# Performance work log

Hardware: AMD Instinct MI355X
Metric: run time of the kernel (lower is better)

Reference implementation:

```python
import jax, jax.numpy as jnp
import numpy as np


def setup_inputs() -> dict:
    key = jax.random.key(0)
    k1, k2, k3 = jax.random.split(key, 3)
    B, H, S, D = 2, 16, 2048, 64
    q = jax.random.normal(k1, (B, H, S, D), dtype=jnp.float32)
    k = jax.random.normal(k2, (B, H, S, D), dtype=jnp.float32)
    v = jax.random.normal(k3, (B, H, S, D), dtype=jnp.float32)
    return {"q": q, "k": k, "v": v}


def reference(q, k, v):
    orig_dtype = q.dtype
    q = q.astype(jnp.float32)
    k = k.astype(jnp.float32)
    v = v.astype(jnp.float32)
    B, H, S, D = q.shape
    # Per-head fixed decay rate: s_h = log2(1 - 2^(-5-h))
    head_idx = jnp.arange(H, dtype=jnp.float32)
    s = jnp.log2(1.0 - jnp.exp2(-5.0 - head_idx))  # [H]
    pos = jnp.arange(S, dtype=jnp.float32)
    pos_diff = pos[:, None] - pos[None, :]  # [S, S], i - j
    # Decay matrix n[h,i,j] = 2^((i-j)*s_h), masked to causal (i >= j)
    n = jnp.exp2(pos_diff[None, :, :] * s[:, None, None])  # [H, S, S]
    causal = (pos[:, None] >= pos[None, :]).astype(jnp.float32)  # [S, S]
    n = n * causal[None, :, :]
    scale = D ** (-0.5)
    attn = jnp.einsum('bhqd,bhkd->bhqk', q * scale, k)  # [B,H,S,S]
    attn = attn * n[None]
    o = jnp.einsum('bhqk,bhkd->bhqd', attn, v)
    return o.astype(orig_dtype)
```

## Files before the change

### kernel.cpp

```cpp
#include <hip/hip_runtime.h>


#define S_LEN 2048
#define DHEAD 64
#define CHUNK 64
#define NC    32
#define BH    32
#define LDK   72

typedef float  f32x4  __attribute__((ext_vector_type(4)));
typedef short  bf16x8 __attribute__((ext_vector_type(8)));
typedef unsigned short u16x8 __attribute__((ext_vector_type(8)));
typedef unsigned short u16x4 __attribute__((ext_vector_type(4)));

static __device__ __forceinline__ unsigned short f2bf(float f) {
    unsigned int u = __float_as_uint(f);
    u += 0x7FFFu + ((u >> 16) & 1u);
    return (unsigned short)(u >> 16);
}
static __device__ __forceinline__ float bf2f(unsigned short h) {
    return __uint_as_float((unsigned int)h << 16);
}

__global__ __launch_bounds__(256)
void ret_p12(const float* __restrict__ kg, const float* __restrict__ vg,
             unsigned short* __restrict__ Lg, unsigned short* __restrict__ Tg) {
    const int g  = (int)blockIdx.x, bh = (int)blockIdx.y, h = bh & 15;
    const int tid = (int)threadIdx.x;
    const int wv = tid >> 6, ln = tid & 63, quad = ln >> 4, lnlo = ln & 15;
    const float sh   = log2f(1.0f - exp2f(-5.0f - (float)h));
    const float lamC = exp2f(sh * (float)CHUNK);

    __shared__ __align__(16) unsigned short Kt[CHUNK * LDK];
    __shared__ __align__(16) unsigned short Vt[CHUNK * LDK];

    const size_t bb = (size_t)bh * S_LEN * DHEAD;

    float rk[2][8], rv[2][8];
    {
        const size_t cb = bb + (size_t)(4 * g) * CHUNK * DHEAD;
#pragma unroll
        for (int i2 = 0; i2 < 2; ++i2) {
            const int pos0 = wv * 8 + i2 * 32;
            const float* pK = kg + cb + (size_t)pos0 * DHEAD + ln;
            const float* pV = vg + cb + (size_t)pos0 * DHEAD + ln;
#pragma unroll
            for (int j = 0; j < 8; ++j) {
                rk[i2][j] = pK[(size_t)j * DHEAD];
                rv[i2][j] = pV[(size_t)j * DHEAD];
            }
        }
    }

    f32x4 Sreg[4];
#pragma unroll
    for (int nt = 0; nt < 4; ++nt) Sreg[nt] = (f32x4){0.f, 0.f, 0.f, 0.f};

    for (int i = 0; i < 4; ++i) {
        const int c = 4 * g + i;
        if (i) {
            unsigned short* lp = Lg + ((size_t)(bh * NC + c) << 12);
#pragma unroll
            for (int nt = 0; nt < 4; ++nt) {
                u16x4 w;
#pragma unroll
                for (int r = 0; r < 4; ++r) w[r] = f2bf(Sreg[nt][r]);
                *(u16x4*)&lp[(nt * 16 + lnlo) * 64 + wv * 16 + quad * 4] = w;
            }
        }
        if (g == 7 && i == 3) break;

#pragma unroll
        for (int i2 = 0; i2 < 2; ++i2) {
            const int pos0 = wv * 8 + i2 * 32;
            u16x8 tk, tv;
#pragma unroll
            for (int j = 0; j < 8; ++j) {
                const float w = exp2f(sh * (float)(CHUNK - pos0 - j));
                tk[j] = f2bf(rk[i2][j] * w);
                tv[j] = f2bf(rv[i2][j]);
            }
            *(u16x8*)&Kt[ln * LDK + pos0] = tk;
            *(u16x8*)&Vt[ln * LDK + pos0] = tv;
        }
        __syncthreads();

        if (i < 3 && !(g == 7 && i == 2)) {
            const size_t cb = bb + (size_t)(c + 1) * CHUNK * DHEAD;
#pragma unroll
            for (int i2 = 0; i2 < 2; ++i2) {
                const int pos0 = wv * 8 + i2 * 32;
                const float* pK = kg + cb + (size_t)pos0 * DHEAD + ln;
                const float* pV = vg + cb + (size_t)pos0 * DHEAD + ln;
#pragma unroll
                for (int j = 0; j < 8; ++j) {
                    rk[i2][j] = pK[(size_t)j * DHEAD];
                    rv[i2][j] = pV[(size_t)j * DHEAD];
                }
            }
        }

        bf16x8 aK[2];
#pragma unroll
        for (int ks = 0; ks < 2; ++ks)
            aK[ks] = *(const bf16x8*)&Kt[(wv * 16 + lnlo) * LDK + ks * 32 + quad * 8];
#pragma unroll
        for (int nt = 0; nt < 4; ++nt) {
            f32x4 acc = (f32x4){0.f, 0.f, 0.f, 0.f};
#pragma unroll
            for (int ks = 0; ks < 2; ++ks) {
                const bf16x8 bv = *(const bf16x8*)&Vt[(nt * 16 + lnlo) * LDK + ks * 32 + quad * 8];
                acc = __builtin_amdgcn_mfma_f32_16x16x32_bf16(aK[ks], bv, acc, 0, 0, 0);
            }
#pragma unroll
            for (int r = 0; r < 4; ++r) Sreg[nt][r] = lamC * Sreg[nt][r] + acc[r];
        }
        __syncthreads();
    }

    if (g < 7) {
        unsigned short* tp = Tg + ((size_t)(bh * 8 + g) << 12);
#pragma unroll
        for (int nt = 0; nt < 4; ++nt) {
            u16x4 w;
#pragma unroll
            for (int r = 0; r < 4; ++r) w[r] = f2bf(Sreg[nt][r]);
            *(u16x4*)&tp[(nt * 16 + lnlo) * 64 + wv * 16 + quad * 4] = w;
        }
    }
}

__global__ __launch_bounds__(256)
void ret_p3(const float* __restrict__ qg, const float* __restrict__ kg,
            const float* __restrict__ vg, const unsigned short* __restrict__ Lg,
            const unsigned short* __restrict__ Tg, float* __restrict__ og) {
    const int c  = (int)blockIdx.x, bh = (int)blockIdx.y, h = bh & 15;
    const int tid = (int)threadIdx.x;
    const int wv = tid >> 6, ln = tid & 63, quad = ln >> 4, lnlo = ln & 15;
    const float sh    = log2f(1.0f - exp2f(-5.0f - (float)h));
    const float scale = 0.125f;

    __shared__ __align__(16) unsigned short smem[3 * CHUNK * LDK];
    unsigned short* const Ks  = smem;
    unsigned short* const Vt  = smem + CHUNK * LDK;
    unsigned short* const ShL = smem + 2 * CHUNK * LDK;

    const size_t cb = (size_t)bh * S_LEN * DHEAD + (size_t)c * CHUNK * DHEAD;
    const float* qp = qg + cb;
    const float* kp = kg + cb;
    const float* vp = vg + cb;
    float*       op = og + cb;

    {
        const int kr = tid >> 2, kc0 = (tid & 3) * 16;
        const float* p = kp + (size_t)kr * DHEAD + kc0;
        const f32x4 x0 = *(const f32x4*)(p + 0);
        const f32x4 x1 = *(const f32x4*)(p + 4);
        const f32x4 x2 = *(const f32x4*)(p + 8);
        const f32x4 x3 = *(const f32x4*)(p + 12);
        u16x8 w0, w1;
        w0[0]=f2bf(x0[0]); w0[1]=f2bf(x0[1]); w0[2]=f2bf(x0[2]); w0[3]=f2bf(x0[3]);
        w0[4]=f2bf(x1[0]); w0[5]=f2bf(x1[1]); w0[6]=f2bf(x1[2]); w0[7]=f2bf(x1[3]);
        w1[0]=f2bf(x2[0]); w1[1]=f2bf(x2[1]); w1[2]=f2bf(x2[2]); w1[3]=f2bf(x2[3]);
        w1[4]=f2bf(x3[0]); w1[5]=f2bf(x3[1]); w1[6]=f2bf(x3[2]); w1[7]=f2bf(x3[3]);
        *(u16x8*)&Ks[kr * LDK + kc0]     = w0;
        *(u16x8*)&Ks[kr * LDK + kc0 + 8] = w1;
    }
#pragma unroll
    for (int i = 0; i < 2; ++i) {
        const int pos0 = wv * 8 + i * 32;
        const float* p = vp + (size_t)pos0 * DHEAD + ln;
        u16x8 t;
#pragma unroll
        for (int j = 0; j < 8; ++j) t[j] = f2bf(p[(size_t)j * DHEAD]);
        *(u16x8*)&Vt[ln * LDK + pos0] = t;
    }
    {
        const int g = c >> 2;
        const int r = tid >> 2, ccol = (tid & 3) * 16;
        float accS[16];
        if (c & 3) {
            const unsigned short* lp = Lg + ((size_t)(bh * NC + c) << 12) + (size_t)tid * 16;
            const u16x8 a0 = *(const u16x8*)lp;
            const u16x8 a1 = *(const u16x8*)(lp + 8);
#pragma unroll
            for (int j = 0; j < 8; ++j) { accS[j] = bf2f(a0[j]); accS[8 + j] = bf2f(a1[j]); }
        } else {
#pragma unroll
            for (int j = 0; j < 16; ++j) accS[j] = 0.f;
        }
        for (int gp = 0; gp < g; ++gp) {
            const float w = exp2f(sh * (float)(CHUNK * (c - 4 * gp - 4)));
            const unsigned short* tp = Tg + ((size_t)(bh * 8 + gp) << 12) + (size_t)tid * 16;
            const u16x8 t0 = *(const u16x8*)tp;
            const u16x8 t1 = *(const u16x8*)(tp + 8);
#pragma unroll
            for (int j = 0; j < 8; ++j) { accS[j] += w * bf2f(t0[j]); accS[8 + j] += w * bf2f(t1[j]); }
        }
        u16x8 w0, w1;
#pragma unroll
        for (int j = 0; j < 8; ++j) { w0[j] = f2bf(accS[j]); w1[j] = f2bf(accS[8 + j]); }
        *(u16x8*)&ShL[r * LDK + ccol]     = w0;
        *(u16x8*)&ShL[r * LDK + ccol + 8] = w1;
    }

    bf16x8 aQ[2];
    {
        const float* qrow = qp + (size_t)(wv * 16 + lnlo) * DHEAD;
#pragma unroll
        for (int ks = 0; ks < 2; ++ks) {
            const float* p = qrow + ks * 32 + quad * 8;
            bf16x8 a;
#pragma unroll
            for (int j = 0; j < 8; ++j) a[j] = (short)f2bf(p[j]);
            aQ[ks] = a;
        }
    }
    float rf[4];
#pragma unroll
    for (int r = 0; r < 4; ++r) rf[r] = exp2f((float)(wv * 16 + quad * 4 + r) * sh);

    __syncthreads();

    f32x4 o[4];
#pragma unroll
    for (int nt = 0; nt < 4; ++nt) {
        f32x4 a = (f32x4){0.f, 0.f, 0.f, 0.f};
#pragma unroll
        for (int ks = 0; ks < 2; ++ks) {
            const bf16x8 bs = *(const bf16x8*)&ShL[(nt * 16 + lnlo) * LDK + ks * 32 + quad * 8];
            a = __builtin_amdgcn_mfma_f32_16x16x32_bf16(aQ[ks], bs, a, 0, 0, 0);
        }
        o[nt] = a;
    }

    f32x4 acc[4];
#pragma unroll
    for (int nt = 0; nt < 4; ++nt) {
        f32x4 a = (f32x4){0.f, 0.f, 0.f, 0.f};
#pragma unroll
        for (int ks = 0; ks < 2; ++ks) {
            const bf16x8 bk = *(const bf16x8*)&Ks[(nt * 16 + lnlo) * LDK + ks * 32 + quad * 8];
            a = __builtin_amdgcn_mfma_f32_16x16x32_bf16(aQ[ks], bk, a, 0, 0, 0);
        }
        acc[nt] = a;
    }

#pragma unroll
    for (int nt = 0; nt < 4; ++nt)
#pragma unroll
        for (int r = 0; r < 4; ++r) o[nt][r] *= rf[r] * scale;

    __syncthreads();

#pragma unroll
    for (int nt = 0; nt < 4; ++nt) {
        const int jn = nt * 16 + lnlo;
        const float cf = scale * exp2f(-(float)jn * sh);
#pragma unroll
        for (int r = 0; r < 4; ++r) {
            const int ri = wv * 16 + quad * 4 + r;
            float wgt = acc[nt][r] * rf[r] * cf;
            if (ri < jn) wgt = 0.0f;
            ShL[ri * LDK + jn] = f2bf(wgt);
        }
    }
    const bf16x8 aW0 = *(const bf16x8*)&ShL[(wv * 16 + lnlo) * LDK + quad * 8];
    const bf16x8 aW1 = *(const bf16x8*)&ShL[(wv * 16 + lnlo) * LDK + 32 + quad * 8];

#pragma unroll
    for (int nt = 0; nt < 4; ++nt) {
        const bf16x8 bv0 = *(const bf16x8*)&Vt[(nt * 16 + lnlo) * LDK + quad * 8];
        const bf16x8 bv1 = *(const bf16x8*)&Vt[(nt * 16 + lnlo) * LDK + 32 + quad * 8];
        o[nt] = __builtin_amdgcn_mfma_f32_16x16x32_bf16(aW0, bv0, o[nt], 0, 0, 0);
        o[nt] = __builtin_amdgcn_mfma_f32_16x16x32_bf16(aW1, bv1, o[nt], 0, 0, 0);
    }

    __syncthreads();
    float* const Of = (float*)smem;
#pragma unroll
    for (int nt = 0; nt < 4; ++nt)
#pragma unroll
        for (int r = 0; r < 4; ++r)
            Of[(wv * 16 + quad * 4 + r) * 68 + nt * 16 + lnlo] = o[nt][r];
    {
        const int row = tid >> 2, col0 = (tid & 3) * 16;
        const float* src = &Of[row * 68 + col0];
        float* dst = op + (size_t)row * DHEAD + col0;
        *(f32x4*)(dst + 0)  = *(const f32x4*)(src + 0);
        *(f32x4*)(dst + 4)  = *(const f32x4*)(src + 4);
        *(f32x4*)(dst + 8)  = *(const f32x4*)(src + 8);
        *(f32x4*)(dst + 12) = *(const f32x4*)(src + 12);
    }
}

extern "C" void kernel_launch(void* const* d_in, const int* in_sizes, int n_in,
                              void* d_out, int out_size, void* d_ws, size_t ws_size,
                              hipStream_t stream) {
    (void)in_sizes; (void)n_in; (void)out_size; (void)ws_size;
    const float* q = (const float*)d_in[0];
    const float* k = (const float*)d_in[1];
    const float* v = (const float*)d_in[2];
    float* o  = (float*)d_out;
    unsigned short* Lg = (unsigned short*)d_ws;
    unsigned short* Tg = (unsigned short*)((char*)d_ws + (16u << 20));

    dim3 blk(256, 1, 1);
    ret_p12<<<dim3(8, BH, 1), blk, 0, stream>>>(k, v, Lg, Tg);
    ret_p3<<<dim3(NC, BH, 1), blk, 0, stream>>>(q, k, v, Lg, Tg, o);
}
```

Before: 105.6 us.

## Split chunk-state recurrence into parallel per-chunk outer products plus scan kernels

The serial per-group chunk loop in the state kernel is replaced by three kernels. The first computes every chunk's decayed K^T V outer product in parallel (31x32 blocks), the second runs an elementwise intra-group scan producing local prefix states and group totals, and the third scans the group totals so each output block reads one precomputed global prefix instead of looping over all previous groups. This exposes more parallelism in the state phase and cuts redundant reads in the output kernel, at the cost of two extra launches and extra bf16 round trips through global workspace.

```diff
diff --git a/kernel.cpp b/kernel.cpp
--- a/kernel.cpp
+++ b/kernel.cpp
@@ -23,122 +23,129 @@
 }
 
 __global__ __launch_bounds__(256)
-void ret_p12(const float* __restrict__ kg, const float* __restrict__ vg,
-             unsigned short* __restrict__ Lg, unsigned short* __restrict__ Tg) {
-    const int g  = (int)blockIdx.x, bh = (int)blockIdx.y, h = bh & 15;
+void ret_pA(const float* __restrict__ kg, const float* __restrict__ vg,
+            unsigned short* __restrict__ Ug) {
+    const int c  = (int)blockIdx.x, bh = (int)blockIdx.y, h = bh & 15;
     const int tid = (int)threadIdx.x;
     const int wv = tid >> 6, ln = tid & 63, quad = ln >> 4, lnlo = ln & 15;
+    const float sh = log2f(1.0f - exp2f(-5.0f - (float)h));
+
+    __shared__ __align__(16) unsigned short Kt[CHUNK * LDK];
+    __shared__ __align__(16) unsigned short Vt[CHUNK * LDK];
+
+    const size_t cb = (size_t)bh * S_LEN * DHEAD + (size_t)c * CHUNK * DHEAD;
+    const float* kp = kg + cb;
+    const float* vp = vg + cb;
+
+#pragma unroll
+    for (int i = 0; i < 2; ++i) {
+        const int pos0 = wv * 8 + i * 32;
+        const float* pK = kp + (size_t)pos0 * DHEAD + ln;
+        const float* pV = vp + (size_t)pos0 * DHEAD + ln;
+        u16x8 tk, tv;
+#pragma unroll
+        for (int j = 0; j < 8; ++j) {
+            const float w = exp2f(sh * (float)(CHUNK - pos0 - j));
+            tk[j] = f2bf(pK[(size_t)j * DHEAD] * w);
+            tv[j] = f2bf(pV[(size_t)j * DHEAD]);
+        }
+        *(u16x8*)&Kt[ln * LDK + pos0] = tk;
+        *(u16x8*)&Vt[ln * LDK + pos0] = tv;
+    }
+    __syncthreads();
+
+    bf16x8 aK[2];
+#pragma unroll
+    for (int ks = 0; ks < 2; ++ks)
+        aK[ks] = *(const bf16x8*)&Kt[(wv * 16 + lnlo) * LDK + ks * 32 + quad * 8];
+
+    unsigned short* up = Ug + ((size_t)(bh * NC + c) << 12);
+#pragma unroll
+    for (int nt = 0; nt < 4; ++nt) {
+        f32x4 acc = (f32x4){0.f, 0.f, 0.f, 0.f};
+#pragma unroll
+        for (int ks = 0; ks < 2; ++ks) {
+            const bf16x8 bv = *(const bf16x8*)&Vt[(nt * 16 + lnlo) * LDK + ks * 32 + quad * 8];
+            acc = __builtin_amdgcn_mfma_f32_16x16x32_bf16(aK[ks], bv, acc, 0, 0, 0);
+        }
+        u16x4 w;
+#pragma unroll
+        for (int r = 0; r < 4; ++r) w[r] = f2bf(acc[r]);
+        *(u16x4*)&up[(nt * 16 + lnlo) * 64 + wv * 16 + quad * 4] = w;
+    }
+}
+
+__global__ __launch_bounds__(256)
+void ret_pB1(const unsigned short* __restrict__ Ug, unsigned short* __restrict__ Lg,
+             unsigned short* __restrict__ Tg) {
+    const int gx = (int)blockIdx.x, bh = (int)blockIdx.y, h = bh & 15;
+    const int g = gx >> 1, half = gx & 1;
+    const int base = half * 2048 + (int)threadIdx.x * 8;
     const float sh   = log2f(1.0f - exp2f(-5.0f - (float)h));
     const float lamC = exp2f(sh * (float)CHUNK);
 
-    __shared__ __align__(16) unsigned short Kt[CHUNK * LDK];
-    __shared__ __align__(16) unsigned short Vt[CHUNK * LDK];
-
-    const size_t bb = (size_t)bh * S_LEN * DHEAD;
-
-    float rk[2][8], rv[2][8];
-    {
-        const size_t cb = bb + (size_t)(4 * g) * CHUNK * DHEAD;
-#pragma unroll
-        for (int i2 = 0; i2 < 2; ++i2) {
-            const int pos0 = wv * 8 + i2 * 32;
-            const float* pK = kg + cb + (size_t)pos0 * DHEAD + ln;
-            const float* pV = vg + cb + (size_t)pos0 * DHEAD + ln;
-#pragma unroll
-            for (int j = 0; j < 8; ++j) {
-                rk[i2][j] = pK[(size_t)j * DHEAD];
-                rv[i2][j] = pV[(size_t)j * DHEAD];
-            }
-        }
-    }
-
-    f32x4 Sreg[4];
-#pragma unroll
-    for (int nt = 0; nt < 4; ++nt) Sreg[nt] = (f32x4){0.f, 0.f, 0.f, 0.f};
-
-    for (int i = 0; i < 4; ++i) {
-        const int c = 4 * g + i;
-        if (i) {
-            unsigned short* lp = Lg + ((size_t)(bh * NC + c) << 12);
-#pragma unroll
-            for (int nt = 0; nt < 4; ++nt) {
-                u16x4 w;
-#pragma unroll
-                for (int r = 0; r < 4; ++r) w[r] = f2bf(Sreg[nt][r]);
-                *(u16x4*)&lp[(nt * 16 + lnlo) * 64 + wv * 16 + quad * 4] = w;
-            }
-        }
-        if (g == 7 && i == 3) break;
-
-#pragma unroll
-        for (int i2 = 0; i2 < 2; ++i2) {
-            const int pos0 = wv * 8 + i2 * 32;
-            u16x8 tk, tv;
-#pragma unroll
-            for (int j = 0; j < 8; ++j) {
-                const float w = exp2f(sh * (float)(CHUNK - pos0 - j));
-                tk[j] = f2bf(rk[i2][j] * w);
-                tv[j] = f2bf(rv[i2][j]);
-            }
-            *(u16x8*)&Kt[ln * LDK + pos0] = tk;
-            *(u16x8*)&Vt[ln * LDK + pos0] = tv;
-        }
-        __syncthreads();
-
-        if (i < 3 && !(g == 7 && i == 2)) {
-            const size_t cb = bb + (size_t)(c + 1) * CHUNK * DHEAD;
-#pragma unroll
-            for (int i2 = 0; i2 < 2; ++i2) {
-                const int pos0 = wv * 8 + i2 * 32;
-                const float* pK = kg + cb + (size_t)pos0 * DHEAD + ln;
-                const float* pV = vg + cb + (size_t)pos0 * DHEAD + ln;
-#pragma unroll
-                for (int j = 0; j < 8; ++j) {
-                    rk[i2][j] = pK[(size_t)j * DHEAD];
-                    rv[i2][j] = pV[(size_t)j * DHEAD];
-                }
-            }
-        }
-
-        bf16x8 aK[2];
-#pragma unroll
-        for (int ks = 0; ks < 2; ++ks)
-            aK[ks] = *(const bf16x8*)&Kt[(wv * 16 + lnlo) * LDK + ks * 32 + quad * 8];
-#pragma unroll
-        for (int nt = 0; nt < 4; ++nt) {
-            f32x4 acc = (f32x4){0.f, 0.f, 0.f, 0.f};
-#pragma unroll
-            for (int ks = 0; ks < 2; ++ks) {
-                const bf16x8 bv = *(const bf16x8*)&Vt[(nt * 16 + lnlo) * LDK + ks * 32 + quad * 8];
-                acc = __builtin_amdgcn_mfma_f32_16x16x32_bf16(aK[ks], bv, acc, 0, 0, 0);
-            }
-#pragma unroll
-            for (int r = 0; r < 4; ++r) Sreg[nt][r] = lamC * Sreg[nt][r] + acc[r];
-        }
-        __syncthreads();
-    }
-
+    const unsigned short* up = Ug + ((size_t)(bh * NC + 4 * g) << 12) + base;
+    unsigned short*       lp = Lg + ((size_t)(bh * NC + 4 * g) << 12) + base;
+
+    float t[8];
+#pragma unroll
+    for (int i = 0; i < 8; ++i) t[i] = 0.f;
+
+#pragma unroll
+    for (int j = 0; j < 4; ++j) {
+        if (j) {
+            u16x8 w;
+#pragma unroll
+            for (int i = 0; i < 8; ++i) w[i] = f2bf(t[i]);
+            *(u16x8*)(lp + ((size_t)j << 12)) = w;
+        }
+        if (g == 7 && j == 3) break;
+        const u16x8 a = *(const u16x8*)(up + ((size_t)j << 12));
+#pragma unroll
+        for (int i = 0; i < 8; ++i) t[i] = lamC * t[i] + bf2f(a[i]);
+    }
     if (g < 7) {
-        unsigned short* tp = Tg + ((size_t)(bh * 8 + g) << 12);
-#pragma unroll
-        for (int nt = 0; nt < 4; ++nt) {
-            u16x4 w;
-#pragma unroll
-            for (int r = 0; r < 4; ++r) w[r] = f2bf(Sreg[nt][r]);
-            *(u16x4*)&tp[(nt * 16 + lnlo) * 64 + wv * 16 + quad * 4] = w;
-        }
+        u16x8 w;
+#pragma unroll
+        for (int i = 0; i < 8; ++i) w[i] = f2bf(t[i]);
+        *(u16x8*)(Tg + ((size_t)((bh << 3) + g) << 12) + base) = w;
+    }
+}
+
+__global__ __launch_bounds__(256)
+void ret_pB2(const unsigned short* __restrict__ Tg, unsigned short* __restrict__ Gg) {
+    const int half = (int)blockIdx.x, bh = (int)blockIdx.y, h = bh & 15;
+    const int base = half * 2048 + (int)threadIdx.x * 8;
+    const float sh   = log2f(1.0f - exp2f(-5.0f - (float)h));
+    const float lam4 = exp2f(sh * (float)(4 * CHUNK));
+
+    u16x8 tt[7];
+#pragma unroll
+    for (int g = 0; g < 7; ++g)
+        tt[g] = *(const u16x8*)(Tg + ((size_t)((bh << 3) + g) << 12) + base);
+
+    float G[8];
+#pragma unroll
+    for (int i = 0; i < 8; ++i) G[i] = 0.f;
+#pragma unroll
+    for (int g = 0; g < 7; ++g) {
+        u16x8 w;
+#pragma unroll
+        for (int i = 0; i < 8; ++i) { G[i] = lam4 * G[i] + bf2f(tt[g][i]); w[i] = f2bf(G[i]); }
+        *(u16x8*)(Gg + ((size_t)((bh << 3) + g + 1) << 12) + base) = w;
     }
 }
 
 __global__ __launch_bounds__(256)
 void ret_p3(const float* __restrict__ qg, const float* __restrict__ kg,
             const float* __restrict__ vg, const unsigned short* __restrict__ Lg,
-            const unsigned short* __restrict__ Tg, float* __restrict__ og) {
+            const unsigned short* __restrict__ Gg, float* __restrict__ og) {
     const int c  = (int)blockIdx.x, bh = (int)blockIdx.y, h = bh & 15;
     const int tid = (int)threadIdx.x;
     const int wv = tid >> 6, ln = tid & 63, quad = ln >> 4, lnlo = ln & 15;
     const float sh    = log2f(1.0f - exp2f(-5.0f - (float)h));
     const float scale = 0.125f;
+    const int g = c >> 2;
 
     __shared__ __align__(16) unsigned short smem[3 * CHUNK * LDK];
     unsigned short* const Ks  = smem;
@@ -176,7 +183,6 @@
         *(u16x8*)&Vt[ln * LDK + pos0] = t;
     }
     {
-        const int g = c >> 2;
         const int r = tid >> 2, ccol = (tid & 3) * 16;
         float accS[16];
         if (c & 3) {
@@ -189,11 +195,11 @@
 #pragma unroll
             for (int j = 0; j < 16; ++j) accS[j] = 0.f;
         }
-        for (int gp = 0; gp < g; ++gp) {
-            const float w = exp2f(sh * (float)(CHUNK * (c - 4 * gp - 4)));
-            const unsigned short* tp = Tg + ((size_t)(bh * 8 + gp) << 12) + (size_t)tid * 16;
-            const u16x8 t0 = *(const u16x8*)tp;
-            const u16x8 t1 = *(const u16x8*)(tp + 8);
+        if (g) {
+            const float w = exp2f(sh * (float)(CHUNK * (c - 4 * g)));
+            const unsigned short* gp = Gg + ((size_t)((bh << 3) + g) << 12) + (size_t)tid * 16;
+            const u16x8 t0 = *(const u16x8*)gp;
+            const u16x8 t1 = *(const u16x8*)(gp + 8);
 #pragma unroll
             for (int j = 0; j < 8; ++j) { accS[j] += w * bf2f(t0[j]); accS[8 + j] += w * bf2f(t1[j]); }
         }
@@ -302,10 +308,14 @@
     const float* k = (const float*)d_in[1];
     const float* v = (const float*)d_in[2];
     float* o  = (float*)d_out;
-    unsigned short* Lg = (unsigned short*)d_ws;
+    unsigned short* Ug = (unsigned short*)d_ws;
+    unsigned short* Lg = (unsigned short*)((char*)d_ws + ( 8u << 20));
     unsigned short* Tg = (unsigned short*)((char*)d_ws + (16u << 20));
+    unsigned short* Gg = (unsigned short*)((char*)d_ws + (18u << 20));
 
     dim3 blk(256, 1, 1);
-    ret_p12<<<dim3(8, BH, 1), blk, 0, stream>>>(k, v, Lg, Tg);
-    ret_p3<<<dim3(NC, BH, 1), blk, 0, stream>>>(q, k, v, Lg, Tg, o);
-}
+    ret_pA <<<dim3(NC - 1, BH, 1), blk, 0, stream>>>(k, v, Ug);
+    ret_pB1<<<dim3(16, BH, 1),     blk, 0, stream>>>(Ug, Lg, Tg);
+    ret_pB2<<<dim3(2, BH, 1),      blk, 0, stream>>>(Tg, Gg);
+    ret_p3 <<<dim3(NC, BH, 1),     blk, 0, stream>>>(q, k, v, Lg, Gg, o);
+}
```

Measured after the change: 111.2 us. 5.2% more time.

## Halve chunk groups in state pass and hand off bf16 transposed V via workspace

Applied to the files above, without the earlier changes.

The first kernel now processes groups of 2 chunks instead of 4, launching 16 groups per head. This doubles first-kernel parallelism and shortens its serial chain, at the cost of a longer prefix-combine loop in the second kernel. The first kernel also writes the bf16 transposed V tile, XOR-swizzled, to workspace. The second kernel loads that tile directly into LDS with global_load_lds instead of re-reading fp32 V with strided loads and converting it. This trades an extra global write and read of bf16 V for less conversion and transposition work in the output pass.

```diff
diff --git a/kernel.cpp b/kernel.cpp
--- a/kernel.cpp
+++ b/kernel.cpp
@@ -5,6 +5,7 @@
 #define DHEAD 64
 #define CHUNK 64
 #define NC    32
+#define NG    16
 #define BH    32
 #define LDK   72
 
@@ -22,9 +23,14 @@
     return __uint_as_float((unsigned int)h << 16);
 }
 
+#define GLDS16(gp_, lp_) __builtin_amdgcn_global_load_lds( \
+    (const __attribute__((address_space(1))) void*)(gp_),  \
+    (__attribute__((address_space(3))) void*)(lp_), 16, 0, 0)
+
 __global__ __launch_bounds__(256)
 void ret_p12(const float* __restrict__ kg, const float* __restrict__ vg,
-             unsigned short* __restrict__ Lg, unsigned short* __restrict__ Tg) {
+             unsigned short* __restrict__ Ue, unsigned short* __restrict__ Tb,
+             unsigned short* __restrict__ Vr) {
     const int g  = (int)blockIdx.x, bh = (int)blockIdx.y, h = bh & 15;
     const int tid = (int)threadIdx.x;
     const int wv = tid >> 6, ln = tid & 63, quad = ln >> 4, lnlo = ln & 15;
@@ -38,12 +44,12 @@
 
     float rk[2][8], rv[2][8];
     {
-        const size_t cb = bb + (size_t)(4 * g) * CHUNK * DHEAD;
+        const size_t cb0 = bb + (size_t)(2 * g) * CHUNK * DHEAD;
 #pragma unroll
         for (int i2 = 0; i2 < 2; ++i2) {
             const int pos0 = wv * 8 + i2 * 32;
-            const float* pK = kg + cb + (size_t)pos0 * DHEAD + ln;
-            const float* pV = vg + cb + (size_t)pos0 * DHEAD + ln;
+            const float* pK = kg + cb0 + (size_t)pos0 * DHEAD + ln;
+            const float* pV = vg + cb0 + (size_t)pos0 * DHEAD + ln;
 #pragma unroll
             for (int j = 0; j < 8; ++j) {
                 rk[i2][j] = pK[(size_t)j * DHEAD];
@@ -56,20 +62,10 @@
 #pragma unroll
     for (int nt = 0; nt < 4; ++nt) Sreg[nt] = (f32x4){0.f, 0.f, 0.f, 0.f};
 
-    for (int i = 0; i < 4; ++i) {
-        const int c = 4 * g + i;
-        if (i) {
-            unsigned short* lp = Lg + ((size_t)(bh * NC + c) << 12);
-#pragma unroll
-            for (int nt = 0; nt < 4; ++nt) {
-                u16x4 w;
-#pragma unroll
-                for (int r = 0; r < 4; ++r) w[r] = f2bf(Sreg[nt][r]);
-                *(u16x4*)&lp[(nt * 16 + lnlo) * 64 + wv * 16 + quad * 4] = w;
-            }
-        }
-        if (g == 7 && i == 3) break;
-
+#pragma unroll
+    for (int i = 0; i < 2; ++i) {
+        const int c = 2 * g + i;
+        unsigned short* vt = Vr + ((size_t)(bh * NC + c) << 12);
 #pragma unroll
         for (int i2 = 0; i2 < 2; ++i2) {
             const int pos0 = wv * 8 + i2 * 32;
@@ -82,16 +78,18 @@
             }
             *(u16x8*)&Kt[ln * LDK + pos0] = tk;
             *(u16x8*)&Vt[ln * LDK + pos0] = tv;
+            const int ri = (ln * 64 + pos0) ^ ((ln & 7) << 3);
+            *(u16x8*)&vt[ri] = tv;
         }
         __syncthreads();
 
-        if (i < 3 && !(g == 7 && i == 2)) {
-            const size_t cb = bb + (size_t)(c + 1) * CHUNK * DHEAD;
+        if (i == 0) {
+            const size_t cbn = bb + (size_t)(2 * g + 1) * CHUNK * DHEAD;
 #pragma unroll
             for (int i2 = 0; i2 < 2; ++i2) {
                 const int pos0 = wv * 8 + i2 * 32;
-                const float* pK = kg + cb + (size_t)pos0 * DHEAD + ln;
-                const float* pV = vg + cb + (size_t)pos0 * DHEAD + ln;
+                const float* pK = kg + cbn + (size_t)pos0 * DHEAD + ln;
+                const float* pV = vg + cbn + (size_t)pos0 * DHEAD + ln;
 #pragma unroll
                 for (int j = 0; j < 8; ++j) {
                     rk[i2][j] = pK[(size_t)j * DHEAD];
@@ -106,51 +104,66 @@
             aK[ks] = *(const bf16x8*)&Kt[(wv * 16 + lnlo) * LDK + ks * 32 + quad * 8];
 #pragma unroll
         for (int nt = 0; nt < 4; ++nt) {
-            f32x4 acc = (f32x4){0.f, 0.f, 0.f, 0.f};
+            f32x4 a = (f32x4){0.f, 0.f, 0.f, 0.f};
 #pragma unroll
             for (int ks = 0; ks < 2; ++ks) {
                 const bf16x8 bv = *(const bf16x8*)&Vt[(nt * 16 + lnlo) * LDK + ks * 32 + quad * 8];
-                acc = __builtin_amdgcn_mfma_f32_16x16x32_bf16(aK[ks], bv, acc, 0, 0, 0);
-            }
-#pragma unroll
-            for (int r = 0; r < 4; ++r) Sreg[nt][r] = lamC * Sreg[nt][r] + acc[r];
+                a = __builtin_amdgcn_mfma_f32_16x16x32_bf16(aK[ks], bv, a, 0, 0, 0);
+            }
+#pragma unroll
+            for (int r = 0; r < 4; ++r) Sreg[nt][r] = lamC * Sreg[nt][r] + a[r];
         }
         __syncthreads();
-    }
-
-    if (g < 7) {
-        unsigned short* tp = Tg + ((size_t)(bh * 8 + g) << 12);
-#pragma unroll
-        for (int nt = 0; nt < 4; ++nt) {
-            u16x4 w;
-#pragma unroll
-            for (int r = 0; r < 4; ++r) w[r] = f2bf(Sreg[nt][r]);
-            *(u16x4*)&tp[(nt * 16 + lnlo) * 64 + wv * 16 + quad * 4] = w;
+
+        if (i == 0) {
+            unsigned short* up = Ue + ((size_t)(bh * NG + g) << 12);
+#pragma unroll
+            for (int nt = 0; nt < 4; ++nt) {
+                u16x4 w;
+#pragma unroll
+                for (int r = 0; r < 4; ++r) w[r] = f2bf(Sreg[nt][r]);
+                *(u16x4*)&up[(nt * 16 + lnlo) * 64 + wv * 16 + quad * 4] = w;
+            }
+        } else if (g < NG - 1) {
+            unsigned short* tp = Tb + ((size_t)(bh * NG + g) << 12);
+#pragma unroll
+            for (int nt = 0; nt < 4; ++nt) {
+                u16x4 w;
+#pragma unroll
+                for (int r = 0; r < 4; ++r) w[r] = f2bf(Sreg[nt][r]);
+                *(u16x4*)&tp[(nt * 16 + lnlo) * 64 + wv * 16 + quad * 4] = w;
+            }
         }
     }
 }
 
 __global__ __launch_bounds__(256)
 void ret_p3(const float* __restrict__ qg, const float* __restrict__ kg,
-            const float* __restrict__ vg, const unsigned short* __restrict__ Lg,
-            const unsigned short* __restrict__ Tg, float* __restrict__ og) {
+            const unsigned short* __restrict__ Ue, const unsigned short* __restrict__ Tb,
+            const unsigned short* __restrict__ Vr, float* __restrict__ og) {
     const int c  = (int)blockIdx.x, bh = (int)blockIdx.y, h = bh & 15;
     const int tid = (int)threadIdx.x;
     const int wv = tid >> 6, ln = tid & 63, quad = ln >> 4, lnlo = ln & 15;
     const float sh    = log2f(1.0f - exp2f(-5.0f - (float)h));
     const float scale = 0.125f;
-
-    __shared__ __align__(16) unsigned short smem[3 * CHUNK * LDK];
+    const int g = c >> 1;
+
+    __shared__ __align__(16) unsigned short smem[CHUNK * LDK + CHUNK * 64 + CHUNK * LDK];
     unsigned short* const Ks  = smem;
     unsigned short* const Vt  = smem + CHUNK * LDK;
-    unsigned short* const ShL = smem + 2 * CHUNK * LDK;
+    unsigned short* const ShL = smem + CHUNK * LDK + CHUNK * 64;
 
     const size_t cb = (size_t)bh * S_LEN * DHEAD + (size_t)c * CHUNK * DHEAD;
     const float* qp = qg + cb;
     const float* kp = kg + cb;
-    const float* vp = vg + cb;
     float*       op = og + cb;
 
+    {
+        const unsigned short* vt = Vr + ((size_t)(bh * NC + c) << 12);
+        const int wbase = wv * 1024;
+        GLDS16(vt + wbase + ln * 8,       &Vt[wbase]);
+        GLDS16(vt + wbase + 512 + ln * 8, &Vt[wbase + 512]);
+    }
     {
         const int kr = tid >> 2, kc0 = (tid & 3) * 16;
         const float* p = kp + (size_t)kr * DHEAD + kc0;
@@ -166,21 +179,11 @@
         *(u16x8*)&Ks[kr * LDK + kc0]     = w0;
         *(u16x8*)&Ks[kr * LDK + kc0 + 8] = w1;
     }
-#pragma unroll
-    for (int i = 0; i < 2; ++i) {
-        const int pos0 = wv * 8 + i * 32;
-        const float* p = vp + (size_t)pos0 * DHEAD + ln;
-        u16x8 t;
-#pragma unroll
-        for (int j = 0; j < 8; ++j) t[j] = f2bf(p[(size_t)j * DHEAD]);
-        *(u16x8*)&Vt[ln * LDK + pos0] = t;
-    }
-    {
-        const int g = c >> 2;
+    {
         const int r = tid >> 2, ccol = (tid & 3) * 16;
         float accS[16];
-        if (c & 3) {
-            const unsigned short* lp = Lg + ((size_t)(bh * NC + c) << 12) + (size_t)tid * 16;
+        if (c & 1) {
+            const unsigned short* lp = Ue + ((size_t)(bh * NG + g) << 12) + (size_t)tid * 16;
             const u16x8 a0 = *(const u16x8*)lp;
             const u16x8 a1 = *(const u16x8*)(lp + 8);
 #pragma unroll
@@ -190,8 +193,8 @@
             for (int j = 0; j < 16; ++j) accS[j] = 0.f;
         }
         for (int gp = 0; gp < g; ++gp) {
-            const float w = exp2f(sh * (float)(CHUNK * (c - 4 * gp - 4)));
-            const unsigned short* tp = Tg + ((size_t)(bh * 8 + gp) << 12) + (size_t)tid * 16;
+            const float w = exp2f(sh * (float)(CHUNK * (c - 2 * gp - 2)));
+            const unsigned short* tp = Tb + ((size_t)(bh * NG + gp) << 12) + (size_t)tid * 16;
             const u16x8 t0 = *(const u16x8*)tp;
             const u16x8 t1 = *(const u16x8*)(tp + 8);
 #pragma unroll
@@ -270,8 +273,10 @@
 
 #pragma unroll
     for (int nt = 0; nt < 4; ++nt) {
-        const bf16x8 bv0 = *(const bf16x8*)&Vt[(nt * 16 + lnlo) * LDK + quad * 8];
-        const bf16x8 bv1 = *(const bf16x8*)&Vt[(nt * 16 + lnlo) * LDK + 32 + quad * 8];
+        const int row = nt * 16 + lnlo;
+        const int sw  = (row & 7) << 3;
+        const bf16x8 bv0 = *(const bf16x8*)&Vt[(row * 64 + quad * 8) ^ sw];
+        const bf16x8 bv1 = *(const bf16x8*)&Vt[(row * 64 + 32 + quad * 8) ^ sw];
         o[nt] = __builtin_amdgcn_mfma_f32_16x16x32_bf16(aW0, bv0, o[nt], 0, 0, 0);
         o[nt] = __builtin_amdgcn_mfma_f32_16x16x32_bf16(aW1, bv1, o[nt], 0, 0, 0);
     }
@@ -302,10 +307,11 @@
     const float* k = (const float*)d_in[1];
     const float* v = (const float*)d_in[2];
     float* o  = (float*)d_out;
-    unsigned short* Lg = (unsigned short*)d_ws;
-    unsigned short* Tg = (unsigned short*)((char*)d_ws + (16u << 20));
+    unsigned short* Ue = (unsigned short*)d_ws;
+    unsigned short* Tb = (unsigned short*)((char*)d_ws + ( 4u << 20));
+    unsigned short* Vr = (unsigned short*)((char*)d_ws + ( 8u << 20));
 
     dim3 blk(256, 1, 1);
-    ret_p12<<<dim3(8, BH, 1), blk, 0, stream>>>(k, v, Lg, Tg);
-    ret_p3<<<dim3(NC, BH, 1), blk, 0, stream>>>(q, k, v, Lg, Tg, o);
-}
+    ret_p12<<<dim3(NG, BH, 1), blk, 0, stream>>>(k, v, Ue, Tb, Vr);
+    ret_p3 <<<dim3(NC, BH, 1), blk, 0, stream>>>(q, k, Ue, Tb, Vr, o);
+}
```

Result: slower. 109.1 us (+3.3%).
